# Kernel tuning notes

Hardware: AMD Instinct MI355X
Metric: run time of the kernel (lower is better)

## Reference

```python
import jax, jax.numpy as jnp
import numpy as np

D_MODEL = 1024
N_HEADS = 16
D_K = D_MODEL // N_HEADS
SCALE = 1.0 / np.sqrt(D_K).astype(np.float32)
NEG = -1000000000.0


def setup_inputs() -> dict:
    key = jax.random.key(0)
    ks = jax.random.split(key, 5)
    B, S = 2, 2048
    query = jax.random.normal(ks[0], (B, S, D_MODEL), dtype=jnp.float32)
    k_in = jax.random.normal(ks[1], (B, S, D_MODEL), dtype=jnp.float32)
    v_in = jax.random.normal(ks[2], (B, S, D_MODEL), dtype=jnp.float32)
    # causal mask, broadcast over batch and heads; 0 entries get -1e9
    mask = jnp.tril(jnp.ones((S, S), dtype=jnp.int32))[None, None, :, :]
    w_qkv = jax.random.normal(ks[3], (D_MODEL, 3 * D_MODEL), dtype=jnp.float32) * (1.0 / np.sqrt(D_MODEL))
    w_o = jax.random.normal(ks[4], (D_MODEL, D_MODEL), dtype=jnp.float32) * (1.0 / np.sqrt(D_MODEL))
    return {"query": query, "key": k_in, "value": v_in, "mask": mask, "w_qkv": w_qkv, "w_o": w_o}


def reference(query, key, value, mask, w_qkv, w_o):
    # NOTE: original module ignores `key`/`value`; q,k,v all come from `query`.
    B, S, _ = query.shape
    qkv = query @ w_qkv                       # [B,S,3D]
    q, k, v = jnp.split(qkv, 3, axis=-1)
    def heads(x):
        return x.reshape(B, S, N_HEADS, D_K).transpose(0, 2, 1, 3)  # [B,H,S,dk]
    Q, K, V = heads(q), heads(k), heads(v)
    scores = jnp.einsum('bhqd,bhkd->bhqk', Q, K) * SCALE            # [B,H,S,S]
    scores = jnp.where(mask == 0, NEG, scores)
    attn = jax.nn.softmax(scores, axis=-1)
    # Dropout(0.1) treated as eval-mode identity for a deterministic reference.
    context = jnp.einsum('bhqk,bhkd->bhqd', attn, V)                # [B,H,S,dk]
    context = context.transpose(0, 2, 1, 3).reshape(B, S, D_MODEL)
    return context @ w_o
```

## Files before the change

### kernel.cpp

```cpp
#include <hip/hip_runtime.h>
#include <stdint.h>


typedef __attribute__((ext_vector_type(8))) short bf16x8;
typedef __attribute__((ext_vector_type(4))) float f32x4;

#define LOG2E 1.44269504088896340736f
#define QSCALE (0.125f * LOG2E)

__device__ __forceinline__ unsigned short f2b(float f) {
  union { float f; unsigned int i; } x; x.f = f;
  unsigned int i = x.i;
  return (unsigned short)((i + 0x7FFFu + ((i >> 16) & 1u)) >> 16);
}

__device__ __forceinline__ void async16(const void* g, void* l) {
  __builtin_amdgcn_global_load_lds(
      (__attribute__((address_space(1))) void*)g,
      (__attribute__((address_space(3))) void*)l, 16, 0, 0);
}

__device__ __forceinline__ f32x4 mfma16(bf16x8 a, bf16x8 b, f32x4 c) {
  return __builtin_amdgcn_mfma_f32_16x16x32_bf16(a, b, c, 0, 0, 0);
}

__device__ __forceinline__ unsigned int fbits(float f) {
  union { float f; unsigned int i; } x; x.f = f;
  return x.i;
}

__global__ __launch_bounds__(256) void prep(
    const float* __restrict__ X, const float* __restrict__ Wqkv,
    const float* __restrict__ Wo, unsigned short* __restrict__ Xb,
    unsigned short* __restrict__ WqkvT, unsigned short* __restrict__ WoT) {
  __shared__ __align__(16) unsigned short Lt[64 * 64];
  const int bx = blockIdx.x;
  const int t = threadIdx.x;
  if (bx < 2048) {
    const size_t i = ((size_t)bx * 256 + t) * 8;
    float4 a = *(const float4*)(X + i);
    float4 b = *(const float4*)(X + i + 4);
    unsigned short e[8];
    e[0] = f2b(a.x); e[1] = f2b(a.y); e[2] = f2b(a.z); e[3] = f2b(a.w);
    e[4] = f2b(b.x); e[5] = f2b(b.y); e[6] = f2b(b.z); e[7] = f2b(b.w);
    *(uint4*)(Xb + i) = *(const uint4*)e;
    return;
  }
  const bool is_qkv = (bx < 2816);
  const int bid = is_qkv ? bx - 2048 : bx - 2816;
  const float* src = is_qkv ? Wqkv : Wo;
  unsigned short* dst = is_qkv ? WqkvT : WoT;
  const int Ccols = is_qkv ? 3072 : 1024;
  const int r0 = (bid & 15) * 64, c0 = (bid >> 4) * 64;
  const float s = (is_qkv && c0 < 1024) ? QSCALE : 1.0f;
#pragma unroll
  for (int it = 0; it < 4; ++it) {
    int c = it * 256 + t;
    int sr = c >> 4, co = (c & 15) * 4;
    float4 v = *(const float4*)(src + (size_t)(r0 + sr) * Ccols + c0 + co);
    Lt[(co + 0) * 64 + sr] = f2b(v.x * s);
    Lt[(co + 1) * 64 + sr] = f2b(v.y * s);
    Lt[(co + 2) * 64 + sr] = f2b(v.z * s);
    Lt[(co + 3) * 64 + sr] = f2b(v.w * s);
  }
  __syncthreads();
#pragma unroll
  for (int it = 0; it < 2; ++it) {
    int c = it * 256 + t;
    int dr = c >> 3, so = (c & 7) * 8;
    *(uint4*)(dst + (size_t)(c0 + dr) * 1024 + r0 + so) =
        *(const uint4*)(Lt + dr * 64 + so);
  }
}

__global__ __launch_bounds__(256) void gemm_qkv(
    const unsigned short* __restrict__ A, const unsigned short* __restrict__ Bt,
    unsigned short* __restrict__ C, unsigned short* __restrict__ Vt) {
  constexpr int K = 1024, N = 3072;
  __shared__ __align__(16) unsigned short Sm[16896];
  unsigned short* As = Sm;
  unsigned short* Bs = Sm + 8192;
  unsigned short* Lt = Sm;

  const int t = threadIdx.x;
  const int w = t >> 6, l = t & 63;
  const int m0 = blockIdx.y * 128, n0 = blockIdx.x * 128;
  const int wm = (w >> 1) * 64, wn = (w & 1) * 64;
  const int lrow = l & 15, lq = l >> 4;

  f32x4 acc[4][4] = {};

  for (int k0 = 0; k0 < K; k0 += 64) {
    __syncthreads();
#pragma unroll
    for (int r = 0; r < 4; ++r) {
      const int c = r * 256 + t;
      const int row = c >> 3;
      const int so = ((c & 7) ^ (row & 7)) * 8;
      async16(A + (size_t)(m0 + row) * K + k0 + so,
              As + (size_t)(r * 256 + t) * 8);
      async16(Bt + (size_t)(n0 + row) * K + k0 + so,
              Bs + (size_t)(r * 256 + t) * 8);
    }
    asm volatile("s_waitcnt vmcnt(0)" ::: "memory");
    __syncthreads();

#pragma unroll
    for (int kh = 0; kh < 2; ++kh) {
      bf16x8 af[4], bf[4];
      const int phys = ((kh * 4 + lq) ^ (lrow & 7)) * 8;
#pragma unroll
      for (int i = 0; i < 4; ++i)
        af[i] = *(const bf16x8*)(As + (wm + i * 16 + lrow) * 64 + phys);
#pragma unroll
      for (int j = 0; j < 4; ++j)
        bf[j] = *(const bf16x8*)(Bs + (wn + j * 16 + lrow) * 64 + phys);
#pragma unroll
      for (int i = 0; i < 4; ++i)
#pragma unroll
        for (int j = 0; j < 4; ++j)
          acc[i][j] = mfma16(af[i], bf[j], acc[i][j]);
    }
  }

  if (n0 < 2048) {
#pragma unroll
    for (int i = 0; i < 4; ++i)
#pragma unroll
      for (int j = 0; j < 4; ++j)
#pragma unroll
        for (int r = 0; r < 4; ++r) {
          int gr = m0 + wm + i * 16 + lq * 4 + r;
          int gc = n0 + wn + j * 16 + lrow;
          C[(size_t)gr * N + gc] = f2b(acc[i][j][r]);
        }
  } else {
    __syncthreads();
#pragma unroll
    for (int i = 0; i < 4; ++i)
#pragma unroll
      for (int j = 0; j < 4; ++j) {
        int col_loc = wn + j * 16 + lrow;
        int row_loc = wm + i * 16 + lq * 4;
        uint2 pk;
        pk.x = (unsigned int)f2b(acc[i][j][0]) |
               ((unsigned int)f2b(acc[i][j][1]) << 16);
        pk.y = (unsigned int)f2b(acc[i][j][2]) |
               ((unsigned int)f2b(acc[i][j][3]) << 16);
        *(uint2*)(Lt + col_loc * 132 + row_loc) = pk;
      }
    __syncthreads();
    const int b = m0 >> 11, s0 = m0 & 2047;
    const int vb0 = n0 - 2048;
#pragma unroll
    for (int rnd = 0; rnd < 8; ++rnd) {
      int vrow = rnd * 16 + (t >> 4);
      int sloc = (t & 15) * 8;
      int vcol = vb0 + vrow;
      int bh = b * 16 + (vcol >> 6);
      int d = vcol & 63;
      *(uint4*)(Vt + ((size_t)bh * 64 + d) * 2048 + s0 + sloc) =
          *(const uint4*)(Lt + vrow * 132 + sloc);
    }
  }
}

__global__ __launch_bounds__(256) void gemm_o(
    const unsigned short* __restrict__ A, const unsigned short* __restrict__ Bt,
    float* __restrict__ C, int M, int N, int K) {
  __shared__ __align__(16) unsigned short As[64 * 64];
  __shared__ __align__(16) unsigned short Bs[128 * 64];
  const int t = threadIdx.x;
  const int w = t >> 6, l = t & 63;
  const int m0 = blockIdx.y * 64, n0 = blockIdx.x * 128;
  const int wm = (w & 1) * 32, wn = (w >> 1) * 64;
  const int lrow = l & 15, lq = l >> 4;

  f32x4 acc[2][4] = {};

  for (int k0 = 0; k0 < K; k0 += 64) {
    __syncthreads();
#pragma unroll
    for (int r = 0; r < 2; ++r) {
      const int c = r * 256 + t;
      const int row = c >> 3;
      const int so = ((c & 7) ^ (row & 7)) * 8;
      async16(A + (size_t)(m0 + row) * K + k0 + so,
              As + (size_t)(r * 256 + t) * 8);
    }
#pragma unroll
    for (int r = 0; r < 4; ++r) {
      const int c = r * 256 + t;
      const int row = c >> 3;
      const int so = ((c & 7) ^ (row & 7)) * 8;
      async16(Bt + (size_t)(n0 + row) * K + k0 + so,
              Bs + (size_t)(r * 256 + t) * 8);
    }
    asm volatile("s_waitcnt vmcnt(0)" ::: "memory");
    __syncthreads();

#pragma unroll
    for (int kh = 0; kh < 2; ++kh) {
      bf16x8 af[2], bf[4];
      const int phys = ((kh * 4 + lq) ^ (lrow & 7)) * 8;
#pragma unroll
      for (int i = 0; i < 2; ++i)
        af[i] = *(const bf16x8*)(As + (wm + i * 16 + lrow) * 64 + phys);
#pragma unroll
      for (int j = 0; j < 4; ++j)
        bf[j] = *(const bf16x8*)(Bs + (wn + j * 16 + lrow) * 64 + phys);
#pragma unroll
      for (int i = 0; i < 2; ++i)
#pragma unroll
        for (int j = 0; j < 4; ++j)
          acc[i][j] = mfma16(af[i], bf[j], acc[i][j]);
    }
  }

#pragma unroll
  for (int i = 0; i < 2; ++i)
#pragma unroll
    for (int j = 0; j < 4; ++j)
#pragma unroll
      for (int r = 0; r < 4; ++r) {
        int gr = m0 + wm + i * 16 + lq * 4 + r;
        int gc = n0 + wn + j * 16 + lrow;
        C[(size_t)gr * N + gc] = acc[i][j][r];
      }
}

__global__ __launch_bounds__(512, 4) void attn_fwd(
    const unsigned short* __restrict__ qkv,
    const unsigned short* __restrict__ Vt,
    unsigned short* __restrict__ ctx) {
  __shared__ __align__(16) unsigned short Ks[2][64 * 64];
  __shared__ __align__(16) unsigned short Vs[2][64 * 64];
  __shared__ __align__(16) unsigned short Ps[8][16 * 72];

  const int ti = blockIdx.x;
  const int bh = blockIdx.y;
  const int b = bh >> 4, h = bh & 15;
  const int t = threadIdx.x;
  const int g = t >> 8;
  const int tl = t & 255;
  const int w = tl >> 6;
  const int gw = t >> 6;
  const int l = t & 63;
  const int lm = l & 15, lq = l >> 4;
  const int sw = lm & 7;
  const int c0 = (lq ^ sw) * 8;
  const int c1 = ((lq + 4) ^ sw) * 8;

  const int qt0[2] = {ti * 64, (31 - ti) * 64};
  const int ktmax = 31 - ti;
  const int nsup = (ktmax >> 1) + 1;

  const unsigned short* Qp = qkv + (size_t)(b * 2048) * 3072 + h * 64;
  const unsigned short* Kp = qkv + (size_t)(b * 2048) * 3072 + 1024 + h * 64;
  const unsigned short* Vb = Vt + (size_t)bh * 64 * 2048;

  bf16x8 qf[2][2];
#pragma unroll
  for (int qt = 0; qt < 2; ++qt) {
    const int qrow = qt0[qt] + w * 16 + lm;
    qf[qt][0] = *(const bf16x8*)(Qp + (size_t)qrow * 3072 + lq * 8);
    qf[qt][1] = *(const bf16x8*)(Qp + (size_t)qrow * 3072 + 32 + lq * 8);
  }

  f32x4 oacc[2][4] = {};
  float lsum[2] = {0.f, 0.f};

  for (int jj = 0; jj < nsup; ++jj) {
    const int kt = 2 * jj + g;
    const bool have = (kt <= ktmax);
    __syncthreads();
    if (have) {
      const int kk0 = kt * 64;
#pragma unroll
      for (int r = 0; r < 2; ++r) {
        int cl = r * 256 + tl;
        int row = cl >> 3, cp = cl & 7;
        int so = ((cp ^ (row & 7)) * 8);
        async16(Kp + (size_t)(kk0 + row) * 3072 + so,
                Ks[g] + (size_t)(r * 256 + w * 64) * 8);
        async16(Vb + (size_t)row * 2048 + kk0 + so,
                Vs[g] + (size_t)(r * 256 + w * 64) * 8);
      }
    }
    asm volatile("s_waitcnt vmcnt(0)" ::: "memory");
    __syncthreads();
    if (!have) continue;

    const unsigned short* Kc = Ks[g];
    const unsigned short* Vc = Vs[g];

    bf16x8 vf[8];
#pragma unroll
    for (int nt = 0; nt < 4; ++nt) {
      const unsigned short* vr = Vc + (nt * 16 + lm) * 64;
      vf[nt] = *(const bf16x8*)(vr + c0);
      vf[4 + nt] = *(const bf16x8*)(vr + c1);
    }

#pragma unroll
    for (int qt = 0; qt < 2; ++qt) {
      if (qt == 0 && kt > ti) continue;
      f32x4 sacc[4] = {};
#pragma unroll
      for (int mt = 0; mt < 4; ++mt) {
        const unsigned short* kr = Kc + (mt * 16 + lm) * 64;
        bf16x8 bk0 = *(const bf16x8*)(kr + c0);
        bf16x8 bk1 = *(const bf16x8*)(kr + c1);
        sacc[mt] = mfma16(bk0, qf[qt][0], sacc[mt]);
        sacc[mt] = mfma16(bk1, qf[qt][1], sacc[mt]);
      }

      const bool diag = (kt == ((qt == 0) ? ti : ktmax));
      const int qloc = w * 16 + lm;
#pragma unroll
      for (int mt = 0; mt < 4; ++mt) {
        float p0 = __builtin_amdgcn_exp2f(sacc[mt][0]);
        float p1 = __builtin_amdgcn_exp2f(sacc[mt][1]);
        float p2 = __builtin_amdgcn_exp2f(sacc[mt][2]);
        float p3 = __builtin_amdgcn_exp2f(sacc[mt][3]);
        if (diag) {
          const int kvb = mt * 16 + lq * 4;
          if (kvb + 0 > qloc) p0 = 0.f;
          if (kvb + 1 > qloc) p1 = 0.f;
          if (kvb + 2 > qloc) p2 = 0.f;
          if (kvb + 3 > qloc) p3 = 0.f;
        }
        lsum[qt] += (p0 + p1) + (p2 + p3);
        uint2 pk;
        pk.x = (fbits(p1) & 0xFFFF0000u) | (fbits(p0) >> 16);
        pk.y = (fbits(p3) & 0xFFFF0000u) | (fbits(p2) >> 16);
        *(uint2*)(&Ps[gw][lm * 72 + mt * 16 + lq * 4]) = pk;
      }
      asm volatile("s_waitcnt lgkmcnt(0)" ::: "memory");

#pragma unroll
      for (int ks = 0; ks < 2; ++ks) {
        bf16x8 pa = *(const bf16x8*)(&Ps[gw][lm * 72 + ks * 32 + lq * 8]);
#pragma unroll
        for (int nt = 0; nt < 4; ++nt)
          oacc[qt][nt] = mfma16(pa, vf[ks * 4 + nt], oacc[qt][nt]);
      }
    }
  }

#pragma unroll
  for (int qt = 0; qt < 2; ++qt) {
    lsum[qt] += __shfl_xor(lsum[qt], 16, 64);
    lsum[qt] += __shfl_xor(lsum[qt], 32, 64);
  }

  __syncthreads();
  float* fbuf[2] = {(float*)Ks, (float*)Vs};
  float* lbuf = (float*)Ps;
  if (g == 1) {
#pragma unroll
    for (int qt = 0; qt < 2; ++qt) {
#pragma unroll
      for (int nt = 0; nt < 4; ++nt)
#pragma unroll
        for (int r = 0; r < 4; ++r)
          fbuf[qt][(w * 16 + lq * 4 + r) * 64 + nt * 16 + lm] = oacc[qt][nt][r];
      if (l < 16) lbuf[qt * 64 + w * 16 + lm] = lsum[qt];
    }
  }
  __syncthreads();
  if (g == 0) {
#pragma unroll
    for (int qt = 0; qt < 2; ++qt) {
      const float ltot = lsum[qt] + lbuf[qt * 64 + w * 16 + lm];
      float rinv[4];
#pragma unroll
      for (int r = 0; r < 4; ++r)
        rinv[r] = 1.f / __shfl(ltot, lq * 4 + r, 64);
#pragma unroll
      for (int nt = 0; nt < 4; ++nt)
#pragma unroll
        for (int r = 0; r < 4; ++r) {
          float v = oacc[qt][nt][r] +
                    fbuf[qt][(w * 16 + lq * 4 + r) * 64 + nt * 16 + lm];
          size_t tok = (size_t)b * 2048 + qt0[qt] + w * 16 + lq * 4 + r;
          ctx[tok * 1024 + h * 64 + nt * 16 + lm] = f2b(v * rinv[r]);
        }
    }
  }
}

extern "C" void kernel_launch(void* const* d_in, const int* in_sizes, int n_in,
                              void* d_out, int out_size, void* d_ws,
                              size_t ws_size, hipStream_t stream) {
  const float* query = (const float*)d_in[0];
  const float* w_qkv = (const float*)d_in[4];
  const float* w_o = (const float*)d_in[5];
  float* out = (float*)d_out;

  unsigned short* ws = (unsigned short*)d_ws;
  unsigned short* wqkvT = ws;
  unsigned short* woT = wqkvT + (size_t)3072 * 1024;
  unsigned short* Xb = woT + (size_t)1024 * 1024;
  unsigned short* qkv = Xb + (size_t)4096 * 1024;
  unsigned short* Vt = qkv + (size_t)4096 * 3072;
  unsigned short* ctx = Xb;

  prep<<<dim3(3072), 256, 0, stream>>>(query, w_qkv, w_o, Xb, wqkvT, woT);
  gemm_qkv<<<dim3(24, 32), 256, 0, stream>>>(Xb, wqkvT, qkv, Vt);
  attn_fwd<<<dim3(16, 32), 512, 0, stream>>>(qkv, Vt, ctx);
  gemm_o<<<dim3(8, 64), 256, 0, stream>>>(ctx, woT, out, 4096, 1024, 1024);
}
```

Baseline: 205.3 us.

## Load K and V fragments directly from global memory, dropping LDS staging

The attention kernel no longer stages K and V tiles in shared memory through async global-to-LDS copies with per-iteration block barriers. Each wave now loads its MFMA operand fragments for K and V straight from global memory into registers. Each half-block walks its own key tiles independently, with no synchronisation inside the loop. This removes the barriers and the LDS round-trip, but all four waves of a group now load the same K/V data redundantly, relying on cache. The uncoalesced 16-byte strided loads also stay exposed, since nothing prefetches them.

```diff
diff --git a/kernel.cpp b/kernel.cpp
--- a/kernel.cpp
+++ b/kernel.cpp
@@ -233,27 +233,22 @@
     const unsigned short* __restrict__ qkv,
     const unsigned short* __restrict__ Vt,
     unsigned short* __restrict__ ctx) {
-  __shared__ __align__(16) unsigned short Ks[2][64 * 64];
-  __shared__ __align__(16) unsigned short Vs[2][64 * 64];
   __shared__ __align__(16) unsigned short Ps[8][16 * 72];
+  __shared__ __align__(16) float fscr[2][64 * 64];
+  __shared__ float lscr[2][64];
 
   const int ti = blockIdx.x;
   const int bh = blockIdx.y;
   const int b = bh >> 4, h = bh & 15;
   const int t = threadIdx.x;
   const int g = t >> 8;
-  const int tl = t & 255;
-  const int w = tl >> 6;
+  const int w = (t >> 6) & 3;
   const int gw = t >> 6;
   const int l = t & 63;
   const int lm = l & 15, lq = l >> 4;
-  const int sw = lm & 7;
-  const int c0 = (lq ^ sw) * 8;
-  const int c1 = ((lq + 4) ^ sw) * 8;
 
   const int qt0[2] = {ti * 64, (31 - ti) * 64};
   const int ktmax = 31 - ti;
-  const int nsup = (ktmax >> 1) + 1;
 
   const unsigned short* Qp = qkv + (size_t)(b * 2048) * 3072 + h * 64;
   const unsigned short* Kp = qkv + (size_t)(b * 2048) * 3072 + 1024 + h * 64;
@@ -270,36 +265,25 @@
   f32x4 oacc[2][4] = {};
   float lsum[2] = {0.f, 0.f};
 
-  for (int jj = 0; jj < nsup; ++jj) {
-    const int kt = 2 * jj + g;
-    const bool have = (kt <= ktmax);
-    __syncthreads();
-    if (have) {
-      const int kk0 = kt * 64;
-#pragma unroll
-      for (int r = 0; r < 2; ++r) {
-        int cl = r * 256 + tl;
-        int row = cl >> 3, cp = cl & 7;
-        int so = ((cp ^ (row & 7)) * 8);
-        async16(Kp + (size_t)(kk0 + row) * 3072 + so,
-                Ks[g] + (size_t)(r * 256 + w * 64) * 8);
-        async16(Vb + (size_t)row * 2048 + kk0 + so,
-                Vs[g] + (size_t)(r * 256 + w * 64) * 8);
-      }
-    }
-    asm volatile("s_waitcnt vmcnt(0)" ::: "memory");
-    __syncthreads();
-    if (!have) continue;
-
-    const unsigned short* Kc = Ks[g];
-    const unsigned short* Vc = Vs[g];
-
+  const unsigned short* Kl = Kp + (size_t)lm * 3072 + lq * 8;
+  const unsigned short* Vl = Vb + (size_t)lm * 2048 + lq * 8;
+
+  for (int kt = g; kt <= ktmax; kt += 2) {
+    const int kk0 = kt * 64;
+
+    bf16x8 kf[8];
+#pragma unroll
+    for (int mt = 0; mt < 4; ++mt) {
+      const unsigned short* kr = Kl + (size_t)(kk0 + mt * 16) * 3072;
+      kf[2 * mt + 0] = *(const bf16x8*)(kr);
+      kf[2 * mt + 1] = *(const bf16x8*)(kr + 32);
+    }
     bf16x8 vf[8];
 #pragma unroll
     for (int nt = 0; nt < 4; ++nt) {
-      const unsigned short* vr = Vc + (nt * 16 + lm) * 64;
-      vf[nt] = *(const bf16x8*)(vr + c0);
-      vf[4 + nt] = *(const bf16x8*)(vr + c1);
+      const unsigned short* vr = Vl + (size_t)(nt * 16) * 2048 + kk0;
+      vf[nt] = *(const bf16x8*)(vr);
+      vf[4 + nt] = *(const bf16x8*)(vr + 32);
     }
 
 #pragma unroll
@@ -308,11 +292,8 @@
       f32x4 sacc[4] = {};
 #pragma unroll
       for (int mt = 0; mt < 4; ++mt) {
-        const unsigned short* kr = Kc + (mt * 16 + lm) * 64;
-        bf16x8 bk0 = *(const bf16x8*)(kr + c0);
-        bf16x8 bk1 = *(const bf16x8*)(kr + c1);
-        sacc[mt] = mfma16(bk0, qf[qt][0], sacc[mt]);
-        sacc[mt] = mfma16(bk1, qf[qt][1], sacc[mt]);
+        sacc[mt] = mfma16(kf[2 * mt + 0], qf[qt][0], sacc[mt]);
+        sacc[mt] = mfma16(kf[2 * mt + 1], qf[qt][1], sacc[mt]);
       }
 
       const bool diag = (kt == ((qt == 0) ? ti : ktmax));
@@ -355,8 +336,6 @@
   }
 
   __syncthreads();
-  float* fbuf[2] = {(float*)Ks, (float*)Vs};
-  float* lbuf = (float*)Ps;
   if (g == 1) {
 #pragma unroll
     for (int qt = 0; qt < 2; ++qt) {
@@ -364,15 +343,15 @@
       for (int nt = 0; nt < 4; ++nt)
 #pragma unroll
         for (int r = 0; r < 4; ++r)
-          fbuf[qt][(w * 16 + lq * 4 + r) * 64 + nt * 16 + lm] = oacc[qt][nt][r];
-      if (l < 16) lbuf[qt * 64 + w * 16 + lm] = lsum[qt];
+          fscr[qt][(w * 16 + lq * 4 + r) * 64 + nt * 16 + lm] = oacc[qt][nt][r];
+      if (l < 16) lscr[qt][w * 16 + lm] = lsum[qt];
     }
   }
   __syncthreads();
   if (g == 0) {
 #pragma unroll
     for (int qt = 0; qt < 2; ++qt) {
-      const float ltot = lsum[qt] + lbuf[qt * 64 + w * 16 + lm];
+      const float ltot = lsum[qt] + lscr[qt][w * 16 + lm];
       float rinv[4];
 #pragma unroll
       for (int r = 0; r < 4; ++r)
@@ -382,7 +361,7 @@
 #pragma unroll
         for (int r = 0; r < 4; ++r) {
           float v = oacc[qt][nt][r] +
-                    fbuf[qt][(w * 16 + lq * 4 + r) * 64 + nt * 16 + lm];
+                    fscr[qt][(w * 16 + lq * 4 + r) * 64 + nt * 16 + lm];
           size_t tok = (size_t)b * 2048 + qt0[qt] + w * 16 + lq * 4 + r;
           ctx[tok * 1024 + h * 64 + nt * 16 + lm] = f2b(v * rinv[r]);
         }
```

New measurement: 299.5 us. 1.46x slower.

## Restructure causal attention to one query tile per block with double-buffered KV prefetch

Applied to the files above, without the earlier changes.

Drops the paired-query-tile, two-group split-K scheme (512 threads, cross-group reduction through shared memory). Each 256-thread block now handles a single 64-row query tile, launched heaviest-first, and walks all causal KV tiles itself. The next K/V tile is prefetched into the alternate buffer while the current one is computed. The P staging buffer also gets an XOR swizzle in place of padding. This removes the final cross-group reduction and the idle-group imbalance, but the per-block work becomes uneven and is left to the scheduler to balance.

```diff
diff --git a/kernel.cpp b/kernel.cpp
--- a/kernel.cpp
+++ b/kernel.cpp
@@ -229,70 +229,67 @@
       }
 }
 
-__global__ __launch_bounds__(512, 4) void attn_fwd(
+__global__ __launch_bounds__(256, 4) void attn_fwd(
     const unsigned short* __restrict__ qkv,
     const unsigned short* __restrict__ Vt,
     unsigned short* __restrict__ ctx) {
   __shared__ __align__(16) unsigned short Ks[2][64 * 64];
   __shared__ __align__(16) unsigned short Vs[2][64 * 64];
-  __shared__ __align__(16) unsigned short Ps[8][16 * 72];
-
-  const int ti = blockIdx.x;
+  __shared__ __align__(16) unsigned short Ps[4][16 * 64];
+
+  const int qt = 31 - blockIdx.x;
   const int bh = blockIdx.y;
   const int b = bh >> 4, h = bh & 15;
-  const int t = threadIdx.x;
-  const int g = t >> 8;
-  const int tl = t & 255;
-  const int w = tl >> 6;
-  const int gw = t >> 6;
-  const int l = t & 63;
+  const int t = threadIdx.x, w = t >> 6, l = t & 63;
   const int lm = l & 15, lq = l >> 4;
   const int sw = lm & 7;
   const int c0 = (lq ^ sw) * 8;
   const int c1 = ((lq + 4) ^ sw) * 8;
 
-  const int qt0[2] = {ti * 64, (31 - ti) * 64};
-  const int ktmax = 31 - ti;
-  const int nsup = (ktmax >> 1) + 1;
+  const int q0 = qt * 64;
+  const int ktmax = qt;
 
   const unsigned short* Qp = qkv + (size_t)(b * 2048) * 3072 + h * 64;
   const unsigned short* Kp = qkv + (size_t)(b * 2048) * 3072 + 1024 + h * 64;
   const unsigned short* Vb = Vt + (size_t)bh * 64 * 2048;
 
-  bf16x8 qf[2][2];
-#pragma unroll
-  for (int qt = 0; qt < 2; ++qt) {
-    const int qrow = qt0[qt] + w * 16 + lm;
-    qf[qt][0] = *(const bf16x8*)(Qp + (size_t)qrow * 3072 + lq * 8);
-    qf[qt][1] = *(const bf16x8*)(Qp + (size_t)qrow * 3072 + 32 + lq * 8);
-  }
-
-  f32x4 oacc[2][4] = {};
-  float lsum[2] = {0.f, 0.f};
-
-  for (int jj = 0; jj < nsup; ++jj) {
-    const int kt = 2 * jj + g;
-    const bool have = (kt <= ktmax);
-    __syncthreads();
-    if (have) {
-      const int kk0 = kt * 64;
+  const int qrow = q0 + w * 16 + lm;
+  bf16x8 qf0 = *(const bf16x8*)(Qp + (size_t)qrow * 3072 + lq * 8);
+  bf16x8 qf1 = *(const bf16x8*)(Qp + (size_t)qrow * 3072 + 32 + lq * 8);
+
+  f32x4 oacc[4] = {};
+  float lsum = 0.f;
+
+#pragma unroll
+  for (int r = 0; r < 2; ++r) {
+    int cl = r * 256 + t;
+    int row = cl >> 3, cp = cl & 7;
+    int so = ((cp ^ (row & 7)) * 8);
+    async16(Kp + (size_t)row * 3072 + so,
+            Ks[0] + (size_t)(r * 256 + w * 64) * 8);
+    async16(Vb + (size_t)row * 2048 + so,
+            Vs[0] + (size_t)(r * 256 + w * 64) * 8);
+  }
+
+  for (int kt = 0; kt <= ktmax; ++kt) {
+    const int cur = kt & 1;
+    asm volatile("s_waitcnt vmcnt(0)" ::: "memory");
+    __syncthreads();
+    if (kt < ktmax) {
+      const int nk0 = (kt + 1) * 64;
 #pragma unroll
       for (int r = 0; r < 2; ++r) {
-        int cl = r * 256 + tl;
+        int cl = r * 256 + t;
         int row = cl >> 3, cp = cl & 7;
         int so = ((cp ^ (row & 7)) * 8);
-        async16(Kp + (size_t)(kk0 + row) * 3072 + so,
-                Ks[g] + (size_t)(r * 256 + w * 64) * 8);
-        async16(Vb + (size_t)row * 2048 + kk0 + so,
-                Vs[g] + (size_t)(r * 256 + w * 64) * 8);
+        async16(Kp + (size_t)(nk0 + row) * 3072 + so,
+                Ks[cur ^ 1] + (size_t)(r * 256 + w * 64) * 8);
+        async16(Vb + (size_t)row * 2048 + nk0 + so,
+                Vs[cur ^ 1] + (size_t)(r * 256 + w * 64) * 8);
       }
     }
-    asm volatile("s_waitcnt vmcnt(0)" ::: "memory");
-    __syncthreads();
-    if (!have) continue;
-
-    const unsigned short* Kc = Ks[g];
-    const unsigned short* Vc = Vs[g];
+    const unsigned short* Kc = Ks[cur];
+    const unsigned short* Vc = Vs[cur];
 
     bf16x8 vf[8];
 #pragma unroll
@@ -302,92 +299,62 @@
       vf[4 + nt] = *(const bf16x8*)(vr + c1);
     }
 
-#pragma unroll
-    for (int qt = 0; qt < 2; ++qt) {
-      if (qt == 0 && kt > ti) continue;
-      f32x4 sacc[4] = {};
-#pragma unroll
-      for (int mt = 0; mt < 4; ++mt) {
-        const unsigned short* kr = Kc + (mt * 16 + lm) * 64;
-        bf16x8 bk0 = *(const bf16x8*)(kr + c0);
-        bf16x8 bk1 = *(const bf16x8*)(kr + c1);
-        sacc[mt] = mfma16(bk0, qf[qt][0], sacc[mt]);
-        sacc[mt] = mfma16(bk1, qf[qt][1], sacc[mt]);
+    f32x4 sacc[4] = {};
+#pragma unroll
+    for (int mt = 0; mt < 4; ++mt) {
+      const unsigned short* kr = Kc + (mt * 16 + lm) * 64;
+      bf16x8 bk0 = *(const bf16x8*)(kr + c0);
+      bf16x8 bk1 = *(const bf16x8*)(kr + c1);
+      sacc[mt] = mfma16(bk0, qf0, sacc[mt]);
+      sacc[mt] = mfma16(bk1, qf1, sacc[mt]);
+    }
+
+    const bool diag = (kt == ktmax);
+    const int qloc = w * 16 + lm;
+#pragma unroll
+    for (int mt = 0; mt < 4; ++mt) {
+      float p0 = __builtin_amdgcn_exp2f(sacc[mt][0]);
+      float p1 = __builtin_amdgcn_exp2f(sacc[mt][1]);
+      float p2 = __builtin_amdgcn_exp2f(sacc[mt][2]);
+      float p3 = __builtin_amdgcn_exp2f(sacc[mt][3]);
+      if (diag) {
+        const int kvb = mt * 16 + lq * 4;
+        if (kvb + 0 > qloc) p0 = 0.f;
+        if (kvb + 1 > qloc) p1 = 0.f;
+        if (kvb + 2 > qloc) p2 = 0.f;
+        if (kvb + 3 > qloc) p3 = 0.f;
       }
-
-      const bool diag = (kt == ((qt == 0) ? ti : ktmax));
-      const int qloc = w * 16 + lm;
-#pragma unroll
-      for (int mt = 0; mt < 4; ++mt) {
-        float p0 = __builtin_amdgcn_exp2f(sacc[mt][0]);
-        float p1 = __builtin_amdgcn_exp2f(sacc[mt][1]);
-        float p2 = __builtin_amdgcn_exp2f(sacc[mt][2]);
-        float p3 = __builtin_amdgcn_exp2f(sacc[mt][3]);
-        if (diag) {
-          const int kvb = mt * 16 + lq * 4;
-          if (kvb + 0 > qloc) p0 = 0.f;
-          if (kvb + 1 > qloc) p1 = 0.f;
-          if (kvb + 2 > qloc) p2 = 0.f;
-          if (kvb + 3 > qloc) p3 = 0.f;
-        }
-        lsum[qt] += (p0 + p1) + (p2 + p3);
-        uint2 pk;
-        pk.x = (fbits(p1) & 0xFFFF0000u) | (fbits(p0) >> 16);
-        pk.y = (fbits(p3) & 0xFFFF0000u) | (fbits(p2) >> 16);
-        *(uint2*)(&Ps[gw][lm * 72 + mt * 16 + lq * 4]) = pk;
-      }
-      asm volatile("s_waitcnt lgkmcnt(0)" ::: "memory");
-
-#pragma unroll
-      for (int ks = 0; ks < 2; ++ks) {
-        bf16x8 pa = *(const bf16x8*)(&Ps[gw][lm * 72 + ks * 32 + lq * 8]);
-#pragma unroll
-        for (int nt = 0; nt < 4; ++nt)
-          oacc[qt][nt] = mfma16(pa, vf[ks * 4 + nt], oacc[qt][nt]);
-      }
-    }
-  }
-
-#pragma unroll
-  for (int qt = 0; qt < 2; ++qt) {
-    lsum[qt] += __shfl_xor(lsum[qt], 16, 64);
-    lsum[qt] += __shfl_xor(lsum[qt], 32, 64);
-  }
-
-  __syncthreads();
-  float* fbuf[2] = {(float*)Ks, (float*)Vs};
-  float* lbuf = (float*)Ps;
-  if (g == 1) {
-#pragma unroll
-    for (int qt = 0; qt < 2; ++qt) {
+      lsum += (p0 + p1) + (p2 + p3);
+      uint2 pk;
+      pk.x = (fbits(p1) & 0xFFFF0000u) | (fbits(p0) >> 16);
+      pk.y = (fbits(p3) & 0xFFFF0000u) | (fbits(p2) >> 16);
+      *(uint2*)(&Ps[w][lm * 64 + ((mt * 4 + lq) ^ (sw << 1)) * 4]) = pk;
+    }
+    asm volatile("s_waitcnt lgkmcnt(0)" ::: "memory");
+
+#pragma unroll
+    for (int ks = 0; ks < 2; ++ks) {
+      bf16x8 pa =
+          *(const bf16x8*)(&Ps[w][lm * 64 + ((ks * 4 + lq) ^ sw) * 8]);
 #pragma unroll
       for (int nt = 0; nt < 4; ++nt)
-#pragma unroll
-        for (int r = 0; r < 4; ++r)
-          fbuf[qt][(w * 16 + lq * 4 + r) * 64 + nt * 16 + lm] = oacc[qt][nt][r];
-      if (l < 16) lbuf[qt * 64 + w * 16 + lm] = lsum[qt];
-    }
-  }
-  __syncthreads();
-  if (g == 0) {
-#pragma unroll
-    for (int qt = 0; qt < 2; ++qt) {
-      const float ltot = lsum[qt] + lbuf[qt * 64 + w * 16 + lm];
-      float rinv[4];
-#pragma unroll
-      for (int r = 0; r < 4; ++r)
-        rinv[r] = 1.f / __shfl(ltot, lq * 4 + r, 64);
-#pragma unroll
-      for (int nt = 0; nt < 4; ++nt)
-#pragma unroll
-        for (int r = 0; r < 4; ++r) {
-          float v = oacc[qt][nt][r] +
-                    fbuf[qt][(w * 16 + lq * 4 + r) * 64 + nt * 16 + lm];
-          size_t tok = (size_t)b * 2048 + qt0[qt] + w * 16 + lq * 4 + r;
-          ctx[tok * 1024 + h * 64 + nt * 16 + lm] = f2b(v * rinv[r]);
-        }
-    }
-  }
+        oacc[nt] = mfma16(pa, vf[ks * 4 + nt], oacc[nt]);
+    }
+  }
+
+  lsum += __shfl_xor(lsum, 16, 64);
+  lsum += __shfl_xor(lsum, 32, 64);
+
+  float rinv[4];
+#pragma unroll
+  for (int r = 0; r < 4; ++r) rinv[r] = 1.f / __shfl(lsum, lq * 4 + r, 64);
+#pragma unroll
+  for (int nt = 0; nt < 4; ++nt)
+#pragma unroll
+    for (int r = 0; r < 4; ++r) {
+      size_t tok = (size_t)b * 2048 + q0 + w * 16 + lq * 4 + r;
+      ctx[tok * 1024 + h * 64 + nt * 16 + lm] = f2b(oacc[nt][r] * rinv[r]);
+    }
 }
 
 extern "C" void kernel_launch(void* const* d_in, const int* in_sizes, int n_in,
@@ -408,6 +375,6 @@
 
   prep<<<dim3(3072), 256, 0, stream>>>(query, w_qkv, w_o, Xb, wqkvT, woT);
   gemm_qkv<<<dim3(24, 32), 256, 0, stream>>>(Xb, wqkvT, qkv, Vt);
-  attn_fwd<<<dim3(16, 32), 512, 0, stream>>>(qkv, Vt, ctx);
+  attn_fwd<<<dim3(32, 32), 256, 0, stream>>>(qkv, Vt, ctx);
   gemm_o<<<dim3(8, 64), 256, 0, stream>>>(ctx, woT, out, 4096, 1024, 1024);
 }
```

Result: slower. 211.7 us (+3.1%).

## Double-buffer K/V tiles with async prefetch and swizzle P scratch layout

Applied to the files above, without the earlier changes.

Adds a second LDS buffer per K/V tile so the next tile's global-to-LDS loads are issued before computing on the current one. The wait drops from a full vmcnt(0) to vmcnt(4), overlapping load latency with compute, and raw s_barrier replaces __syncthreads. The P scratch buffer loses its padding and uses an XOR swizzle to avoid bank conflicts while shrinking LDS. LDS use doubles for K/V, which may lower occupancy under launch_bounds(512,4), and the epilogue buffers are remapped to fit.

```diff
diff --git a/kernel.cpp b/kernel.cpp
--- a/kernel.cpp
+++ b/kernel.cpp
@@ -233,9 +233,9 @@
     const unsigned short* __restrict__ qkv,
     const unsigned short* __restrict__ Vt,
     unsigned short* __restrict__ ctx) {
-  __shared__ __align__(16) unsigned short Ks[2][64 * 64];
-  __shared__ __align__(16) unsigned short Vs[2][64 * 64];
-  __shared__ __align__(16) unsigned short Ps[8][16 * 72];
+  __shared__ __align__(16) unsigned short Ks[2][2][64 * 64];
+  __shared__ __align__(16) unsigned short Vs[2][2][64 * 64];
+  __shared__ __align__(16) unsigned short Ps[8][16 * 64];
 
   const int ti = blockIdx.x;
   const int bh = blockIdx.y;
@@ -270,29 +270,48 @@
   f32x4 oacc[2][4] = {};
   float lsum[2] = {0.f, 0.f};
 
+  {
+    const int kk0 = g * 64;
+#pragma unroll
+    for (int r = 0; r < 2; ++r) {
+      int cl = r * 256 + tl;
+      int row = cl >> 3, cp = cl & 7;
+      int so = ((cp ^ (row & 7)) * 8);
+      async16(Kp + (size_t)(kk0 + row) * 3072 + so,
+              Ks[g][0] + (size_t)(r * 256 + w * 64) * 8);
+      async16(Vb + (size_t)row * 2048 + kk0 + so,
+              Vs[g][0] + (size_t)(r * 256 + w * 64) * 8);
+    }
+  }
+
   for (int jj = 0; jj < nsup; ++jj) {
     const int kt = 2 * jj + g;
+    const int cur = jj & 1;
     const bool have = (kt <= ktmax);
-    __syncthreads();
-    if (have) {
-      const int kk0 = kt * 64;
+    const bool pref = (kt + 2 <= ktmax);
+
+    asm volatile("s_barrier" ::: "memory");
+    if (pref) {
+      const int nk0 = (kt + 2) * 64;
 #pragma unroll
       for (int r = 0; r < 2; ++r) {
         int cl = r * 256 + tl;
         int row = cl >> 3, cp = cl & 7;
         int so = ((cp ^ (row & 7)) * 8);
-        async16(Kp + (size_t)(kk0 + row) * 3072 + so,
-                Ks[g] + (size_t)(r * 256 + w * 64) * 8);
-        async16(Vb + (size_t)row * 2048 + kk0 + so,
-                Vs[g] + (size_t)(r * 256 + w * 64) * 8);
-      }
-    }
-    asm volatile("s_waitcnt vmcnt(0)" ::: "memory");
-    __syncthreads();
+        async16(Kp + (size_t)(nk0 + row) * 3072 + so,
+                Ks[g][cur ^ 1] + (size_t)(r * 256 + w * 64) * 8);
+        async16(Vb + (size_t)row * 2048 + nk0 + so,
+                Vs[g][cur ^ 1] + (size_t)(r * 256 + w * 64) * 8);
+      }
+      asm volatile("s_waitcnt vmcnt(4)" ::: "memory");
+    } else {
+      asm volatile("s_waitcnt vmcnt(0)" ::: "memory");
+    }
+    asm volatile("s_barrier" ::: "memory");
     if (!have) continue;
 
-    const unsigned short* Kc = Ks[g];
-    const unsigned short* Vc = Vs[g];
+    const unsigned short* Kc = Ks[g][cur];
+    const unsigned short* Vc = Vs[g][cur];
 
     bf16x8 vf[8];
 #pragma unroll
@@ -334,13 +353,14 @@
         uint2 pk;
         pk.x = (fbits(p1) & 0xFFFF0000u) | (fbits(p0) >> 16);
         pk.y = (fbits(p3) & 0xFFFF0000u) | (fbits(p2) >> 16);
-        *(uint2*)(&Ps[gw][lm * 72 + mt * 16 + lq * 4]) = pk;
+        *(uint2*)(&Ps[gw][lm * 64 + ((mt * 4 + lq) ^ (sw << 1)) * 4]) = pk;
       }
       asm volatile("s_waitcnt lgkmcnt(0)" ::: "memory");
 
 #pragma unroll
       for (int ks = 0; ks < 2; ++ks) {
-        bf16x8 pa = *(const bf16x8*)(&Ps[gw][lm * 72 + ks * 32 + lq * 8]);
+        bf16x8 pa =
+            *(const bf16x8*)(&Ps[gw][lm * 64 + ((ks * 4 + lq) ^ sw) * 8]);
 #pragma unroll
         for (int nt = 0; nt < 4; ++nt)
           oacc[qt][nt] = mfma16(pa, vf[ks * 4 + nt], oacc[qt][nt]);
@@ -355,8 +375,8 @@
   }
 
   __syncthreads();
-  float* fbuf[2] = {(float*)Ks, (float*)Vs};
-  float* lbuf = (float*)Ps;
+  float* fbuf[2] = {(float*)(&Ks[0][0][0]), (float*)(&Ks[0][0][0]) + 4096};
+  float* lbuf = (float*)(&Vs[0][0][0]);
   if (g == 1) {
 #pragma unroll
     for (int qt = 0; qt < 2; ++qt) {
```

Result: slower. 213.5 us (+4.0%).
